# Performance work log

Measured on AMD Instinct MI355X. Metric: run time of the kernel, lower is better.

## Reference

```python
import jax, jax.numpy as jnp
import numpy as np

N = 16384      # nodes
E = 131072     # edges
L = 256        # latent size
H = 256        # mlp hidden size
S = 4          # message passing steps
OUT = 128      # decoder node output size
EPS = 1e-6     # flax LayerNorm epsilon


def _mlp(x, W0, b0, W1, b1):
    h = jax.nn.relu(x @ W0 + b0)
    return h @ W1 + b1


def _mlp_ln(x, W0, b0, W1, b1, ls, lb):
    y = _mlp(x, W0, b0, W1, b1)
    mu = y.mean(-1, keepdims=True)
    var = ((y - mu) ** 2).mean(-1, keepdims=True)
    return (y - mu) * jax.lax.rsqrt(var + EPS) * ls + lb


def setup_inputs() -> dict:
    key = jax.random.key(0)
    ks = iter(jax.random.split(key, 64))
    std = 0.02

    def w(shape):
        return jax.random.normal(next(ks), shape, dtype=jnp.float32) * std

    inp = {
        'node_feats': jax.random.normal(next(ks), (N, 3), dtype=jnp.float32),
        'edge_feats': jax.random.normal(next(ks), (E, 4), dtype=jnp.float32),
        'senders': jax.random.randint(next(ks), (E,), 0, N, dtype=jnp.int32),
        'receivers': jax.random.randint(next(ks), (E,), 0, N, dtype=jnp.int32),
        # node embedder MLP (3 -> H -> L) + LayerNorm
        'en_W0': w((3, H)), 'en_b0': jnp.zeros((H,)), 'en_W1': w((H, L)), 'en_b1': jnp.zeros((L,)),
        'en_ls': jnp.ones((L,)), 'en_lb': jnp.zeros((L,)),
        # edge embedder MLP (4 -> H -> L) + LayerNorm
        'ee_W0': w((4, H)), 'ee_b0': jnp.zeros((H,)), 'ee_W1': w((H, L)), 'ee_b1': jnp.zeros((L,)),
        'ee_ls': jnp.ones((L,)), 'ee_lb': jnp.zeros((L,)),
        # processor edge MLPs, stacked over S steps (3L -> H -> L) + LN
        'pe_W0': w((S, 3 * L, H)), 'pe_b0': jnp.zeros((S, H)), 'pe_W1': w((S, H, L)), 'pe_b1': jnp.zeros((S, L)),
        'pe_ls': jnp.ones((S, L)), 'pe_lb': jnp.zeros((S, L)),
        # processor node MLPs, stacked over S steps (2L -> H -> L) + LN
        'pn_W0': w((S, 2 * L, H)), 'pn_b0': jnp.zeros((S, H)), 'pn_W1': w((S, H, L)), 'pn_b1': jnp.zeros((S, L)),
        'pn_ls': jnp.ones((S, L)), 'pn_lb': jnp.zeros((S, L)),
        # node decoder MLP (L -> H -> OUT), no LayerNorm
        'dn_W0': w((L, H)), 'dn_b0': jnp.zeros((H,)), 'dn_W1': w((H, OUT)), 'dn_b1': jnp.zeros((OUT,)),
    }
    return inp


def reference(node_feats, edge_feats, senders, receivers,
              en_W0, en_b0, en_W1, en_b1, en_ls, en_lb,
              ee_W0, ee_b0, ee_W1, ee_b1, ee_ls, ee_lb,
              pe_W0, pe_b0, pe_W1, pe_b1, pe_ls, pe_lb,
              pn_W0, pn_b0, pn_W1, pn_b1, pn_ls, pn_lb,
              dn_W0, dn_b0, dn_W1, dn_b1):
    # Embed raw node/edge features into latent space.
    nodes = _mlp_ln(node_feats, en_W0, en_b0, en_W1, en_b1, en_ls, en_lb)   # [N, L]
    edges = _mlp_ln(edge_feats, ee_W0, ee_b0, ee_W1, ee_b1, ee_ls, ee_lb)   # [E, L]

    def step(carry, p):
        nodes, edges = carry
        (eW0, eb0, eW1, eb1, els, elb, nW0, nb0, nW1, nb1, nls, nlb) = p
        # Edge update: MLP on [edge, sender_node, receiver_node].
        ein = jnp.concatenate([edges, nodes[senders], nodes[receivers]], axis=-1)  # [E, 3L]
        new_e = _mlp_ln(ein, eW0, eb0, eW1, eb1, els, elb)                          # [E, L]
        # Aggregate new edge messages into receiver nodes (segment_sum).
        agg = jax.ops.segment_sum(new_e, receivers, num_segments=N)                # [N, L]
        # Node update: MLP on [node, aggregated messages].
        nin = jnp.concatenate([nodes, agg], axis=-1)                                # [N, 2L]
        new_n = _mlp_ln(nin, nW0, nb0, nW1, nb1, nls, nlb)                          # [N, L]
        # Residual connections (as in DeepTypedGraphNet processor).
        return (nodes + new_n, edges + new_e), None

    (nodes, edges), _ = jax.lax.scan(
        step, (nodes, edges),
        (pe_W0, pe_b0, pe_W1, pe_b1, pe_ls, pe_lb,
         pn_W0, pn_b0, pn_W1, pn_b1, pn_ls, pn_lb))

    # Decoder on nodes (no LayerNorm on the output head).
    out = _mlp(nodes, dn_W0, dn_b0, dn_W1, dn_b1)  # [N, OUT]
    return out
```

## Files before the change

kernel.cpp:

```cpp
#include <hip/hip_runtime.h>
#include <hip/hip_bf16.h>

#define NN 16384
#define NE 131072
#define L 256
#define SSTEPS 4
#define OUTD 128

typedef __attribute__((ext_vector_type(8))) short bf16x8;
typedef __attribute__((ext_vector_type(4))) float f32x4;

typedef const unsigned __attribute__((address_space(1)))* as1_u32p;
typedef unsigned __attribute__((address_space(3)))* as3_u32p;

__device__ __forceinline__ void gload16(const void* g, void* lds) {
  __builtin_amdgcn_global_load_lds((as1_u32p)g, (as3_u32p)lds, 16, 0, 0);
}

__device__ __forceinline__ short f2bs(float f) {
  unsigned u = __builtin_bit_cast(unsigned, f);
  u = (u + 0x7fffu + ((u >> 16) & 1u)) >> 16;
  return (short)u;
}
__device__ __forceinline__ float bs2f(short s) {
  unsigned u = ((unsigned)(unsigned short)s) << 16;
  return __builtin_bit_cast(float, u);
}
__device__ __forceinline__ unsigned cvt_pk_bf16(float lo, float hi) {
  unsigned r;
  asm("v_cvt_pk_bf16_f32 %0, %1, %2" : "=v"(r) : "v"(lo), "v"(hi));
  return r;
}
__device__ __forceinline__ bf16x8 pack_bf16x8(const float v[8]) {
  union { unsigned u[4]; bf16x8 b; } r;
#pragma unroll
  for (int k = 0; k < 4; ++k) r.u[k] = cvt_pk_bf16(v[2 * k], v[2 * k + 1]);
  return r.b;
}

__device__ __forceinline__ void store_tile(short* hs, int l, int mi, int nb,
                                           f32x4 v) {
  const int lm = l & 15, g = l >> 4;
#pragma unroll
  for (int i = 0; i < 4; ++i) {
    const float part = __shfl_xor(v[i], 1);
    if ((l & 1) == 0) {
      const int row = mi * 16 + g * 4 + i;
      const int col = nb + lm;
      const int off = (row * 512 + col * 2) ^ ((row & 7) << 4);
      *(unsigned*)((char*)hs + off) = cvt_pk_bf16(v[i], part);
    }
  }
}

template <int MI, int NT, int KC, int AST>
__device__ __forceinline__ void gemm_lds(const short* __restrict__ Wp,
                                         int Ncols, const short* hs, int n0,
                                         int l, f32x4 acc[MI][NT]) {
  const int lm = l & 15, g = l >> 4;
#pragma unroll
  for (int kc = 0; kc < KC; ++kc) {
    bf16x8 a[MI];
#pragma unroll
    for (int mi = 0; mi < MI; ++mi) {
      const int row = mi * 16 + lm;
      const int off = (row * AST + kc * 64 + g * 16) ^ ((row & 7) << 4);
      a[mi] = *(const bf16x8*)((const char*)hs + off);
    }
#pragma unroll
    for (int ni = 0; ni < NT; ++ni) {
      const int n = n0 + ni * 16 + lm;
      bf16x8 b = *(const bf16x8*)(Wp + ((size_t)kc * Ncols + n) * 32 + g * 8);
#pragma unroll
      for (int mi = 0; mi < MI; ++mi)
        acc[mi][ni] =
            __builtin_amdgcn_mfma_f32_16x16x32_bf16(a[mi], b, acc[mi][ni], 0, 0, 0);
    }
  }
}

__global__ void pack_w(const float* __restrict__ src, short* __restrict__ dst,
                       int K, int N, int cnt) {
  const size_t total = (size_t)K * N * cnt;
  for (size_t i = (size_t)blockIdx.x * blockDim.x + threadIdx.x; i < total;
       i += (size_t)gridDim.x * blockDim.x) {
    const size_t mat = i / ((size_t)K * N);
    const int rem = (int)(i - mat * (size_t)K * N);
    const int k = rem / N, n = rem - k * N;
    dst[mat * (size_t)K * N + ((size_t)(k >> 5) * N + n) * 32 + (k & 31)] =
        f2bs(src[i]);
  }
}

__global__ void pack_w0_pad(const float* __restrict__ src,
                            short* __restrict__ dst, int Kreal) {
  const int i = blockIdx.x * 256 + threadIdx.x;
  if (i >= 256 * 32) return;
  const int n = i >> 5, k = i & 31;
  dst[n * 32 + k] = (k < Kreal) ? f2bs(src[k * 256 + n]) : (short)0;
}

__device__ __forceinline__ void stage_tile256(const short* __restrict__ src0,
                                              short* As, int w, int l) {
#pragma unroll
  for (int i = 0; i < 4; ++i) {
    const int rbase = w * 8 + i * 2;
    const int r = rbase + (l >> 5);
    const int boff = ((l & 31) * 16) ^ ((r & 7) << 4);
    gload16((const char*)(src0 + (size_t)r * L) + boff, As + rbase * 256);
  }
}

__device__ __forceinline__ void stage_nodes_half16(
    const short* __restrict__ a_src, short* As, int w, int l, int n0) {
#pragma unroll
  for (int i = 0; i < 4; ++i) {
    const int r = w * 4 + i;
    if (l < 32) {
      const int cb = (l * 16) ^ ((r & 7) << 4);
      gload16((const char*)(a_src + (size_t)(n0 + r) * L) + cb, As + r * 512);
    }
  }
}

__global__ void csr_hist(const int* __restrict__ recv, int* __restrict__ deg) {
  const int e = blockIdx.x * 256 + threadIdx.x;
  atomicAdd(&deg[recv[e]], 1);
}
__global__ __launch_bounds__(256) void csr_scan(const int* __restrict__ deg,
                                                int* __restrict__ start,
                                                int* __restrict__ cursor) {
  __shared__ int part[256];
  const int t = threadIdx.x;
  int s = 0;
  for (int i = 0; i < NN / 256; ++i) s += deg[t * (NN / 256) + i];
  part[t] = s;
  __syncthreads();
  if (t == 0) {
    int acc = 0;
    for (int i = 0; i < 256; ++i) {
      const int v = part[i];
      part[i] = acc;
      acc += v;
    }
  }
  __syncthreads();
  int acc = part[t];
  for (int i = 0; i < NN / 256; ++i) {
    const int n = t * (NN / 256) + i;
    start[n] = acc;
    cursor[n] = acc;
    acc += deg[n];
  }
  if (t == 255) start[NN] = acc;
}
__global__ void csr_scatter(const int* __restrict__ recv,
                            int* __restrict__ cursor, int* __restrict__ elist) {
  const int e = blockIdx.x * 256 + threadIdx.x;
  const int p = atomicAdd(&cursor[recv[e]], 1);
  elist[p] = e;
}
__global__ void csr_sort(const int* __restrict__ start, int* __restrict__ elist) {
  const int n = blockIdx.x * blockDim.x + threadIdx.x;
  if (n >= NN) return;
  const int b = start[n], e = start[n + 1];
  for (int i = b + 1; i < e; ++i) {
    const int v = elist[i];
    int j = i - 1;
    while (j >= b && elist[j] > v) {
      elist[j + 1] = elist[j];
      --j;
    }
    elist[j + 1] = v;
  }
}

__device__ __forceinline__ void ln_row(const short* smem, int row, int seg,
                                       const float lsv[16], const float lbv[16],
                                       float ne[16]) {
  const int off0 = (row * 512 + seg * 16) ^ ((row & 7) << 4);
  const int off1 = (row * 512 + 256 + seg * 16) ^ ((row & 7) << 4);
  const bf16x8 y0 = *(const bf16x8*)((const char*)smem + off0);
  const bf16x8 y1 = *(const bf16x8*)((const char*)smem + off1);
  float v[16];
#pragma unroll
  for (int k = 0; k < 8; ++k) {
    v[k] = bs2f(y0[k]);
    v[8 + k] = bs2f(y1[k]);
  }
  float s = 0.f;
#pragma unroll
  for (int k = 0; k < 16; ++k) s += v[k];
#pragma unroll
  for (int o = 1; o < 16; o <<= 1) s += __shfl_xor(s, o);
  const float mu = s * (1.f / 256.f);
  float sq = 0.f;
#pragma unroll
  for (int k = 0; k < 16; ++k) {
    const float d = v[k] - mu;
    sq += d * d;
  }
#pragma unroll
  for (int o = 1; o < 16; o <<= 1) sq += __shfl_xor(sq, o);
  const float rstd = rsqrtf(sq * (1.f / 256.f) + 1e-6f);
#pragma unroll
  for (int k = 0; k < 16; ++k) ne[k] = (v[k] - mu) * rstd * lsv[k] + lbv[k];
}

__device__ __forceinline__ void load16(const float* __restrict__ p, int seg,
                                       float d[16]) {
  const float4 a0 = *(const float4*)(p + seg * 8);
  const float4 a1 = *(const float4*)(p + seg * 8 + 4);
  const float4 a2 = *(const float4*)(p + 128 + seg * 8);
  const float4 a3 = *(const float4*)(p + 128 + seg * 8 + 4);
  d[0] = a0.x; d[1] = a0.y; d[2] = a0.z; d[3] = a0.w;
  d[4] = a1.x; d[5] = a1.y; d[6] = a1.z; d[7] = a1.w;
  d[8] = a2.x; d[9] = a2.y; d[10] = a2.z; d[11] = a2.w;
  d[12] = a3.x; d[13] = a3.y; d[14] = a3.z; d[15] = a3.w;
}

__global__ __launch_bounds__(256, 4) void proj_mfma(
    const short* __restrict__ nodes_b, const short* __restrict__ Wfull,
    short* __restrict__ NSb, short* __restrict__ NRb) {
  __shared__ char smem[16384];
  short* As = (short*)smem;
  const int t = threadIdx.x, w = t >> 6, l = t & 63;
  const int tr = t >> 4, seg = t & 15;
  const int n0 = blockIdx.x * 32;
  const short* Wp = Wfull + (size_t)(8 + blockIdx.y * 8) * 256 * 32;
  short* out = blockIdx.y ? NRb : NSb;

  stage_tile256(nodes_b + (size_t)n0 * L, As, w, l);
  __syncthreads();

  f32x4 acc[2][4] = {};
  gemm_lds<2, 4, 8, 512>(Wp, L, As, w * 64, l, acc);
  __syncthreads();
#pragma unroll
  for (int ni = 0; ni < 4; ++ni)
#pragma unroll
    for (int mi = 0; mi < 2; ++mi)
      store_tile(As, l, mi, w * 64 + ni * 16, acc[mi][ni]);
  __syncthreads();

#pragma unroll
  for (int p = 0; p < 2; ++p) {
    const int row = p * 16 + tr;
    const int off0 = (row * 512 + seg * 16) ^ ((row & 7) << 4);
    const int off1 = (row * 512 + 256 + seg * 16) ^ ((row & 7) << 4);
    *(bf16x8*)(out + (size_t)(n0 + row) * L + seg * 8) =
        *(const bf16x8*)((const char*)As + off0);
    *(bf16x8*)(out + (size_t)(n0 + row) * L + 128 + seg * 8) =
        *(const bf16x8*)((const char*)As + off1);
  }
}

__global__ __launch_bounds__(256, 4) void edge_step_mfma(
    const short* __restrict__ NSb, const short* __restrict__ NRb,
    short* __restrict__ edges_b, short* __restrict__ new_e,
    const int* __restrict__ senders, const int* __restrict__ receivers,
    const short* __restrict__ W0p, const float* __restrict__ b0,
    const short* __restrict__ W1p, const float* __restrict__ b1,
    const float* __restrict__ ls, const float* __restrict__ lb) {
  __shared__ char smem[32768];
  short* As = (short*)smem;
  short* nsrB = (short*)(smem + 16384);
  const int t = threadIdx.x, w = t >> 6, l = t & 63;
  const int lm = l & 15, g = l >> 4;
  const int tr = t >> 4, seg = t & 15;
  const int e0 = blockIdx.x * 32;

  const int sn0 = senders[e0 + tr], rc0 = receivers[e0 + tr];
  const int sn1 = senders[e0 + 16 + tr], rc1 = receivers[e0 + 16 + tr];
  stage_tile256(edges_b + (size_t)e0 * L, As, w, l);
  __syncthreads();

  bf16x8 gn[2][2], gr[2][2];
  {
    const short* p0 = NSb + (size_t)sn0 * L + seg * 8;
    gn[0][0] = *(const bf16x8*)p0;
    gn[0][1] = *(const bf16x8*)(p0 + 128);
    const short* p1 = NSb + (size_t)sn1 * L + seg * 8;
    gn[1][0] = *(const bf16x8*)p1;
    gn[1][1] = *(const bf16x8*)(p1 + 128);
    const short* q0 = NRb + (size_t)rc0 * L + seg * 8;
    gr[0][0] = *(const bf16x8*)q0;
    gr[0][1] = *(const bf16x8*)(q0 + 128);
    const short* q1 = NRb + (size_t)rc1 * L + seg * 8;
    gr[1][0] = *(const bf16x8*)q1;
    gr[1][1] = *(const bf16x8*)(q1 + 128);
  }

  f32x4 acc[2][4] = {};
  gemm_lds<2, 4, 8, 512>(W0p, L, As, w * 64, l, acc);

  bf16x8 old0[2], old1[2];
#pragma unroll
  for (int p = 0; p < 2; ++p) {
    const int row = p * 16 + tr;
    old0[p] = *(const bf16x8*)((const char*)As +
                               ((row * 512 + seg * 16) ^ ((row & 7) << 4)));
    old1[p] = *(const bf16x8*)((const char*)As +
                               ((row * 512 + 256 + seg * 16) ^ ((row & 7) << 4)));
  }

#pragma unroll
  for (int p = 0; p < 2; ++p) {
    const int row = p * 16 + tr;
    float s[16];
#pragma unroll
    for (int k = 0; k < 8; ++k) {
      s[k] = bs2f(gn[p][0][k]) + bs2f(gr[p][0][k]);
      s[8 + k] = bs2f(gn[p][1][k]) + bs2f(gr[p][1][k]);
    }
    const int off0 = (row * 512 + seg * 16) ^ ((row & 7) << 4);
    const int off1 = (row * 512 + 256 + seg * 16) ^ ((row & 7) << 4);
    *(bf16x8*)((char*)nsrB + off0) = pack_bf16x8(s);
    *(bf16x8*)((char*)nsrB + off1) = pack_bf16x8(s + 8);
  }
  __syncthreads();

#pragma unroll
  for (int ni = 0; ni < 4; ++ni) {
    const float bia = b0[w * 64 + ni * 16 + lm];
    const int col = w * 64 + ni * 16 + lm;
#pragma unroll
    for (int mi = 0; mi < 2; ++mi) {
      f32x4 v = acc[mi][ni];
#pragma unroll
      for (int i = 0; i < 4; ++i) {
        const int row = mi * 16 + g * 4 + i;
        const int noff = (row * 512 + col * 2) ^ ((row & 7) << 4);
        v[i] = fmaxf(v[i] + bia + bs2f(*(const short*)((const char*)nsrB + noff)),
                     0.f);
      }
      store_tile(As, l, mi, w * 64 + ni * 16, v);
    }
  }
  __syncthreads();

  f32x4 acc2[2][4] = {};
  gemm_lds<2, 4, 8, 512>(W1p, L, As, w * 64, l, acc2);
#pragma unroll
  for (int ni = 0; ni < 4; ++ni) {
    const float bia = b1[w * 64 + ni * 16 + lm];
#pragma unroll
    for (int mi = 0; mi < 2; ++mi) {
      f32x4 v = acc2[mi][ni];
#pragma unroll
      for (int i = 0; i < 4; ++i) v[i] += bia;
      store_tile(nsrB, l, mi, w * 64 + ni * 16, v);
    }
  }
  __syncthreads();

  float lsv[16], lbv[16];
  load16(ls, seg, lsv);
  load16(lb, seg, lbv);
#pragma unroll
  for (int p = 0; p < 2; ++p) {
    const int row = p * 16 + tr;
    float ne[16];
    ln_row(nsrB, row, seg, lsv, lbv, ne);
    const size_t e = (size_t)(e0 + row);
    *(bf16x8*)(new_e + e * L + seg * 8) = pack_bf16x8(ne);
    *(bf16x8*)(new_e + e * L + 128 + seg * 8) = pack_bf16x8(ne + 8);
    float r0[8], r1[8];
#pragma unroll
    for (int k = 0; k < 8; ++k) {
      r0[k] = bs2f(old0[p][k]) + ne[k];
      r1[k] = bs2f(old1[p][k]) + ne[8 + k];
    }
    *(bf16x8*)(edges_b + e * L + seg * 8) = pack_bf16x8(r0);
    *(bf16x8*)(edges_b + e * L + 128 + seg * 8) = pack_bf16x8(r1);
  }
}

__global__ __launch_bounds__(256, 4) void node_step_mfma(
    float* __restrict__ nodes_f, short* __restrict__ nodes_b,
    const short* __restrict__ new_e, const int* __restrict__ start,
    const int* __restrict__ elist, const short* __restrict__ W0p,
    const float* __restrict__ b0, const short* __restrict__ W1p,
    const float* __restrict__ b1, const float* __restrict__ ls,
    const float* __restrict__ lb, const short* __restrict__ W0nS,
    const short* __restrict__ W0nR, short* __restrict__ NSb,
    short* __restrict__ NRb) {
  __shared__ char smem[16384];
  short* As = (short*)smem;
  short* hb = (short*)smem;
  short* yb = (short*)(smem + 8192);
  const int t = threadIdx.x, w = t >> 6, l = t & 63;
  const int lm = l & 15;
  const int tr = t >> 4, seg = t & 15;
  const int n0 = blockIdx.x * 16;

  stage_nodes_half16(nodes_b, As, w, l, n0);

  {
    const int grp = t >> 5, lc = t & 31;
#pragma unroll
    for (int i = 0; i < 2; ++i) {
      const int r = grp * 2 + i;
      const int n = n0 + r;
      const int b = start[n], e = start[n + 1];
      float acc[8] = {0.f, 0.f, 0.f, 0.f, 0.f, 0.f, 0.f, 0.f};
      if (b < e) {
        bf16x8 v = *(const bf16x8*)(new_e + (size_t)elist[b] * L + lc * 8);
        for (int j = b + 1; j < e; ++j) {
          const bf16x8 nx =
              *(const bf16x8*)(new_e + (size_t)elist[j] * L + lc * 8);
#pragma unroll
          for (int k = 0; k < 8; ++k) acc[k] += bs2f(v[k]);
          v = nx;
        }
#pragma unroll
        for (int k = 0; k < 8; ++k) acc[k] += bs2f(v[k]);
      }
      const int off = (r * 1024 + 512 + lc * 16) ^ ((r & 7) << 4);
      *(bf16x8*)((char*)As + off) = pack_bf16x8(acc);
    }
  }
  __syncthreads();

  f32x4 acc[1][4] = {};
  gemm_lds<1, 4, 16, 1024>(W0p, L, As, w * 64, l, acc);
  __syncthreads();

#pragma unroll
  for (int ni = 0; ni < 4; ++ni) {
    const float bia = b0[w * 64 + ni * 16 + lm];
    f32x4 v = acc[0][ni];
#pragma unroll
    for (int i = 0; i < 4; ++i) v[i] = fmaxf(v[i] + bia, 0.f);
    store_tile(hb, l, 0, w * 64 + ni * 16, v);
  }
  __syncthreads();

  f32x4 acc2[1][4] = {};
  gemm_lds<1, 4, 8, 512>(W1p, L, hb, w * 64, l, acc2);
  __syncthreads();
#pragma unroll
  for (int ni = 0; ni < 4; ++ni) {
    const float bia = b1[w * 64 + ni * 16 + lm];
    f32x4 v = acc2[0][ni];
#pragma unroll
    for (int i = 0; i < 4; ++i) v[i] += bia;
    store_tile(yb, l, 0, w * 64 + ni * 16, v);
  }
  __syncthreads();

  float lsv[16], lbv[16];
  load16(ls, seg, lsv);
  load16(lb, seg, lbv);
  {
    const int row = tr;
    float ne[16];
    ln_row(yb, row, seg, lsv, lbv, ne);
    const size_t n = (size_t)(n0 + row);
    float* nf = nodes_f + n * L;
    float fv[16];
    load16(nf, seg, fv);
    float nv[16];
#pragma unroll
    for (int k = 0; k < 16; ++k) nv[k] = fv[k] + ne[k];
    *(float4*)(nf + seg * 8) = make_float4(nv[0], nv[1], nv[2], nv[3]);
    *(float4*)(nf + seg * 8 + 4) = make_float4(nv[4], nv[5], nv[6], nv[7]);
    *(float4*)(nf + 128 + seg * 8) = make_float4(nv[8], nv[9], nv[10], nv[11]);
    *(float4*)(nf + 128 + seg * 8 + 4) = make_float4(nv[12], nv[13], nv[14], nv[15]);
    const bf16x8 nb0 = pack_bf16x8(nv);
    const bf16x8 nb1 = pack_bf16x8(nv + 8);
    *(bf16x8*)(nodes_b + n * L + seg * 8) = nb0;
    *(bf16x8*)(nodes_b + n * L + 128 + seg * 8) = nb1;
    const int off0 = (row * 512 + seg * 16) ^ ((row & 7) << 4);
    const int off1 = (row * 512 + 256 + seg * 16) ^ ((row & 7) << 4);
    *(bf16x8*)((char*)hb + off0) = nb0;
    *(bf16x8*)((char*)hb + off1) = nb1;
  }

  if (W0nS == nullptr) return;
  __syncthreads();

  {
    f32x4 pa[1][4] = {};
    gemm_lds<1, 4, 8, 512>(W0nS, L, hb, w * 64, l, pa);
#pragma unroll
    for (int ni = 0; ni < 4; ++ni)
      store_tile(yb, l, 0, w * 64 + ni * 16, pa[0][ni]);
    __syncthreads();
    {
      const int row = tr;
      const int off0 = (row * 512 + seg * 16) ^ ((row & 7) << 4);
      const int off1 = (row * 512 + 256 + seg * 16) ^ ((row & 7) << 4);
      *(bf16x8*)(NSb + (size_t)(n0 + row) * L + seg * 8) =
          *(const bf16x8*)((const char*)yb + off0);
      *(bf16x8*)(NSb + (size_t)(n0 + row) * L + 128 + seg * 8) =
          *(const bf16x8*)((const char*)yb + off1);
    }
  }
  __syncthreads();

  {
    f32x4 pa[1][4] = {};
    gemm_lds<1, 4, 8, 512>(W0nR, L, hb, w * 64, l, pa);
#pragma unroll
    for (int ni = 0; ni < 4; ++ni)
      store_tile(yb, l, 0, w * 64 + ni * 16, pa[0][ni]);
    __syncthreads();
    {
      const int row = tr;
      const int off0 = (row * 512 + seg * 16) ^ ((row & 7) << 4);
      const int off1 = (row * 512 + 256 + seg * 16) ^ ((row & 7) << 4);
      *(bf16x8*)(NRb + (size_t)(n0 + row) * L + seg * 8) =
          *(const bf16x8*)((const char*)yb + off0);
      *(bf16x8*)(NRb + (size_t)(n0 + row) * L + 128 + seg * 8) =
          *(const bf16x8*)((const char*)yb + off1);
    }
  }
}

template <int K1, bool WF32>
__global__ __launch_bounds__(256) void embed_mfma(
    const float* __restrict__ x, const short* __restrict__ W0p,
    const float* __restrict__ b0, const short* __restrict__ W1p,
    const float* __restrict__ b1, const float* __restrict__ ls,
    const float* __restrict__ lb, float* __restrict__ dst_f,
    short* __restrict__ dst_b) {
  __shared__ short hs[64 * 256];
  __shared__ short xsb[64 * 32];
  const int t = threadIdx.x, w = t >> 6, l = t & 63;
  const int lm = l & 15, g = l >> 4;
  const int tr = t >> 4, seg = t & 15;
  const int r0 = blockIdx.x * 64;

  if (t < 64) {
    const float* xr = x + (size_t)(r0 + t) * K1;
    float v[8] = {0.f, 0.f, 0.f, 0.f, 0.f, 0.f, 0.f, 0.f};
#pragma unroll
    for (int k = 0; k < K1; ++k) v[k] = xr[k];
    bf16x8 z;
#pragma unroll
    for (int k = 0; k < 8; ++k) z[k] = 0;
    char* rb = (char*)xsb + t * 64;
    *(bf16x8*)(rb + (0 ^ ((t & 3) << 4))) = pack_bf16x8(v);
#pragma unroll
    for (int gi = 1; gi < 4; ++gi) *(bf16x8*)(rb + ((gi * 16) ^ ((t & 3) << 4))) = z;
  }
  __syncthreads();

  f32x4 acc[4][4] = {};
  {
    bf16x8 a[4];
#pragma unroll
    for (int mi = 0; mi < 4; ++mi) {
      const int row = mi * 16 + lm;
      a[mi] = *(const bf16x8*)((const char*)xsb + row * 64 +
                               ((g * 16) ^ ((row & 3) << 4)));
    }
#pragma unroll
    for (int ni = 0; ni < 4; ++ni) {
      const int n = w * 64 + ni * 16 + lm;
      bf16x8 b = *(const bf16x8*)(W0p + n * 32 + g * 8);
#pragma unroll
      for (int mi = 0; mi < 4; ++mi)
        acc[mi][ni] =
            __builtin_amdgcn_mfma_f32_16x16x32_bf16(a[mi], b, acc[mi][ni], 0, 0, 0);
    }
  }
#pragma unroll
  for (int ni = 0; ni < 4; ++ni) {
    const float bia = b0[w * 64 + ni * 16 + lm];
#pragma unroll
    for (int mi = 0; mi < 4; ++mi) {
      f32x4 v = acc[mi][ni];
#pragma unroll
      for (int i = 0; i < 4; ++i) v[i] = fmaxf(v[i] + bia, 0.f);
      store_tile(hs, l, mi, w * 64 + ni * 16, v);
    }
  }
  __syncthreads();

  f32x4 acc2[4][4] = {};
  gemm_lds<4, 4, 8, 512>(W1p, L, hs, w * 64, l, acc2);
  __syncthreads();
#pragma unroll
  for (int ni = 0; ni < 4; ++ni) {
    const float bia = b1[w * 64 + ni * 16 + lm];
#pragma unroll
    for (int mi = 0; mi < 4; ++mi) {
      f32x4 v = acc2[mi][ni];
#pragma unroll
      for (int i = 0; i < 4; ++i) v[i] += bia;
      store_tile(hs, l, mi, w * 64 + ni * 16, v);
    }
  }
  __syncthreads();

  float lsv[16], lbv[16];
  load16(ls, seg, lsv);
  load16(lb, seg, lbv);
#pragma unroll
  for (int p = 0; p < 4; ++p) {
    const int row = p * 16 + tr;
    float ne[16];
    ln_row(hs, row, seg, lsv, lbv, ne);
    const size_t n = (size_t)(r0 + row);
    *(bf16x8*)(dst_b + n * L + seg * 8) = pack_bf16x8(ne);
    *(bf16x8*)(dst_b + n * L + 128 + seg * 8) = pack_bf16x8(ne + 8);
    if (WF32) {
      float* df = dst_f + n * L;
      *(float4*)(df + seg * 8) = make_float4(ne[0], ne[1], ne[2], ne[3]);
      *(float4*)(df + seg * 8 + 4) = make_float4(ne[4], ne[5], ne[6], ne[7]);
      *(float4*)(df + 128 + seg * 8) = make_float4(ne[8], ne[9], ne[10], ne[11]);
      *(float4*)(df + 128 + seg * 8 + 4) =
          make_float4(ne[12], ne[13], ne[14], ne[15]);
    }
  }
}

__global__ __launch_bounds__(256) void decoder_mfma(
    const short* __restrict__ nodes_b, const short* __restrict__ W0p,
    const float* __restrict__ b0, const short* __restrict__ W1p,
    const float* __restrict__ b1, float* __restrict__ out) {
  __shared__ short hs[64 * 256];
  const int t = threadIdx.x, w = t >> 6, l = t & 63;
  const int lm = l & 15, g = l >> 4;
  const int n0 = blockIdx.x * 64;

  const short* baseA[4];
#pragma unroll
  for (int mi = 0; mi < 4; ++mi)
    baseA[mi] = nodes_b + (size_t)(n0 + mi * 16 + lm) * L;

  f32x4 acc[4][4] = {};
#pragma unroll
  for (int kc = 0; kc < 8; ++kc) {
    const int koff = kc * 32 + g * 8;
    bf16x8 a[4];
#pragma unroll
    for (int mi = 0; mi < 4; ++mi) a[mi] = *(const bf16x8*)(baseA[mi] + koff);
#pragma unroll
    for (int ni = 0; ni < 4; ++ni) {
      const int n = w * 64 + ni * 16 + lm;
      bf16x8 b = *(const bf16x8*)(W0p + ((size_t)kc * L + n) * 32 + g * 8);
#pragma unroll
      for (int mi = 0; mi < 4; ++mi)
        acc[mi][ni] = __builtin_amdgcn_mfma_f32_16x16x32_bf16(a[mi], b,
                                                             acc[mi][ni],
                                                             0, 0, 0);
    }
  }
#pragma unroll
  for (int ni = 0; ni < 4; ++ni) {
    const float bia = b0[w * 64 + ni * 16 + lm];
#pragma unroll
    for (int mi = 0; mi < 4; ++mi) {
      f32x4 v = acc[mi][ni];
#pragma unroll
      for (int i = 0; i < 4; ++i) v[i] = fmaxf(v[i] + bia, 0.f);
      store_tile(hs, l, mi, w * 64 + ni * 16, v);
    }
  }
  __syncthreads();

  f32x4 acc2[4][2] = {};
  gemm_lds<4, 2, 8, 512>(W1p, OUTD, hs, w * 32, l, acc2);

  float b14[2];
#pragma unroll
  for (int ni = 0; ni < 2; ++ni) b14[ni] = b1[w * 32 + ni * 16 + lm];
#pragma unroll
  for (int mi = 0; mi < 4; ++mi)
#pragma unroll
    for (int ni = 0; ni < 2; ++ni)
#pragma unroll
      for (int i = 0; i < 4; ++i) {
        const int row = n0 + mi * 16 + g * 4 + i;
        const int col = w * 32 + ni * 16 + lm;
        out[(size_t)row * OUTD + col] = acc2[mi][ni][i] + b14[ni];
      }
}

extern "C" void kernel_launch(void* const* d_in, const int* in_sizes, int n_in,
                              void* d_out, int out_size, void* d_ws,
                              size_t ws_size, hipStream_t stream) {
  const float* node_feats = (const float*)d_in[0];
  const float* edge_feats = (const float*)d_in[1];
  const int* senders = (const int*)d_in[2];
  const int* receivers = (const int*)d_in[3];
  auto f = [&](int i) { return (const float*)d_in[i]; };

  char* p = (char*)d_ws;
  auto alloc = [&](size_t bytes) {
    char* q = p;
    p += (bytes + 255) & ~(size_t)255;
    return q;
  };
  float* nodes_f = (float*)alloc((size_t)NN * L * 4);
  short* nodes_b = (short*)alloc((size_t)NN * L * 2);
  short* edges_b = (short*)alloc((size_t)NE * L * 2);
  short* new_e = (short*)alloc((size_t)NE * L * 2);
  short* NSb = (short*)alloc((size_t)NN * L * 2);
  short* NRb = (short*)alloc((size_t)NN * L * 2);
  int* deg = (int*)alloc((size_t)NN * 4);
  int* start = (int*)alloc((size_t)(NN + 16) * 4);
  int* cursor = (int*)alloc((size_t)NN * 4);
  int* elist = (int*)alloc((size_t)NE * 4);
  short* en_W0p = (short*)alloc(256 * 32 * 2);
  short* ee_W0p = (short*)alloc(256 * 32 * 2);
  short* en_W1p = (short*)alloc(65536 * 2);
  short* ee_W1p = (short*)alloc(65536 * 2);
  short* pe_W0p = (short*)alloc((size_t)4 * 768 * 256 * 2);
  short* pe_W1p = (short*)alloc((size_t)4 * 65536 * 2);
  short* pn_W0p = (short*)alloc((size_t)4 * 512 * 256 * 2);
  short* pn_W1p = (short*)alloc((size_t)4 * 65536 * 2);
  short* dn_W0p = (short*)alloc(65536 * 2);
  short* dn_W1p = (short*)alloc(32768 * 2);

  hipMemsetAsync(deg, 0, (size_t)NN * 4, stream);
  csr_hist<<<NE / 256, 256, 0, stream>>>(receivers, deg);
  csr_scan<<<1, 256, 0, stream>>>(deg, start, cursor);
  csr_scatter<<<NE / 256, 256, 0, stream>>>(receivers, cursor, elist);
  csr_sort<<<NN / 256, 256, 0, stream>>>(start, elist);

  pack_w0_pad<<<32, 256, 0, stream>>>(f(4), en_W0p, 3);
  pack_w0_pad<<<32, 256, 0, stream>>>(f(10), ee_W0p, 4);
  pack_w<<<256, 256, 0, stream>>>(f(6), en_W1p, 256, 256, 1);
  pack_w<<<256, 256, 0, stream>>>(f(12), ee_W1p, 256, 256, 1);
  pack_w<<<1024, 256, 0, stream>>>(f(16), pe_W0p, 768, 256, 4);
  pack_w<<<512, 256, 0, stream>>>(f(18), pe_W1p, 256, 256, 4);
  pack_w<<<1024, 256, 0, stream>>>(f(22), pn_W0p, 512, 256, 4);
  pack_w<<<512, 256, 0, stream>>>(f(24), pn_W1p, 256, 256, 4);
  pack_w<<<256, 256, 0, stream>>>(f(28), dn_W0p, 256, 256, 1);
  pack_w<<<128, 256, 0, stream>>>(f(30), dn_W1p, 256, 128, 1);

  embed_mfma<3, true><<<NN / 64, 256, 0, stream>>>(
      node_feats, en_W0p, f(5), en_W1p, f(7), f(8), f(9), nodes_f, nodes_b);
  embed_mfma<4, false><<<NE / 64, 256, 0, stream>>>(
      edge_feats, ee_W0p, f(11), ee_W1p, f(13), f(14), f(15), nullptr, edges_b);

  for (int s = 0; s < SSTEPS; ++s) {
    const short* W0s = pe_W0p + (size_t)s * 768 * 256;
    if (s == 0)
      proj_mfma<<<dim3(NN / 32, 2), 256, 0, stream>>>(nodes_b, W0s, NSb, NRb);
    edge_step_mfma<<<NE / 32, 256, 0, stream>>>(
        NSb, NRb, edges_b, new_e, senders, receivers, W0s,
        f(17) + (size_t)s * 256, pe_W1p + (size_t)s * 65536,
        f(19) + (size_t)s * 256, f(20) + (size_t)s * 256,
        f(21) + (size_t)s * 256);
    const short* W0n = (s + 1 < SSTEPS) ? pe_W0p + (size_t)(s + 1) * 768 * 256
                                        : nullptr;
    node_step_mfma<<<NN / 16, 256, 0, stream>>>(
        nodes_f, nodes_b, new_e, start, elist,
        pn_W0p + (size_t)s * 512 * 256, f(23) + (size_t)s * 256,
        pn_W1p + (size_t)s * 65536, f(25) + (size_t)s * 256,
        f(26) + (size_t)s * 256, f(27) + (size_t)s * 256,
        W0n ? W0n + (size_t)8 * 256 * 32 : nullptr,
        W0n ? W0n + (size_t)16 * 256 * 32 : nullptr, NSb, NRb);
  }

  decoder_mfma<<<NN / 64, 256, 0, stream>>>(nodes_b, dn_W0p, f(29), dn_W1p,
                                            f(31), (float*)d_out);
}
```

Baseline: 811.1 us.

## Store edges in receiver-sorted order so aggregation reads contiguous rows

Edges are permuted into CSR (receiver-sorted) order once: edge embeddings are gathered through elist, and the sender/receiver arrays are permuted to match. Each edge-step then writes new_e in sorted order, so the node-step segment sum reads contiguous rows instead of indirecting through elist. Edge state stays consistent because it only ever lives in permuted order. This adds a small permutation kernel and an indexed read in the edge embedder.

```diff
diff --git a/kernel.cpp b/kernel.cpp
--- a/kernel.cpp
+++ b/kernel.cpp
@@ -173,6 +173,15 @@
     }
     elist[j + 1] = v;
   }
+}
+__global__ void permute_se(const int* __restrict__ elist,
+                           const int* __restrict__ senders,
+                           const int* __restrict__ receivers,
+                           int* __restrict__ sn_p, int* __restrict__ rc_p) {
+  const int p = blockIdx.x * 256 + threadIdx.x;
+  const int e = elist[p];
+  sn_p[p] = senders[e];
+  rc_p[p] = receivers[e];
 }
 
 __device__ __forceinline__ void ln_row(const short* smem, int row, int seg,
@@ -379,12 +388,11 @@
 __global__ __launch_bounds__(256, 4) void node_step_mfma(
     float* __restrict__ nodes_f, short* __restrict__ nodes_b,
     const short* __restrict__ new_e, const int* __restrict__ start,
-    const int* __restrict__ elist, const short* __restrict__ W0p,
-    const float* __restrict__ b0, const short* __restrict__ W1p,
-    const float* __restrict__ b1, const float* __restrict__ ls,
-    const float* __restrict__ lb, const short* __restrict__ W0nS,
-    const short* __restrict__ W0nR, short* __restrict__ NSb,
-    short* __restrict__ NRb) {
+    const short* __restrict__ W0p, const float* __restrict__ b0,
+    const short* __restrict__ W1p, const float* __restrict__ b1,
+    const float* __restrict__ ls, const float* __restrict__ lb,
+    const short* __restrict__ W0nS, const short* __restrict__ W0nR,
+    short* __restrict__ NSb, short* __restrict__ NRb) {
   __shared__ char smem[16384];
   short* As = (short*)smem;
   short* hb = (short*)smem;
@@ -404,15 +412,8 @@
       const int n = n0 + r;
       const int b = start[n], e = start[n + 1];
       float acc[8] = {0.f, 0.f, 0.f, 0.f, 0.f, 0.f, 0.f, 0.f};
-      if (b < e) {
-        bf16x8 v = *(const bf16x8*)(new_e + (size_t)elist[b] * L + lc * 8);
-        for (int j = b + 1; j < e; ++j) {
-          const bf16x8 nx =
-              *(const bf16x8*)(new_e + (size_t)elist[j] * L + lc * 8);
-#pragma unroll
-          for (int k = 0; k < 8; ++k) acc[k] += bs2f(v[k]);
-          v = nx;
-        }
+      for (int j = b; j < e; ++j) {
+        const bf16x8 v = *(const bf16x8*)(new_e + (size_t)j * L + lc * 8);
 #pragma unroll
         for (int k = 0; k < 8; ++k) acc[k] += bs2f(v[k]);
       }
@@ -520,11 +521,11 @@
 
 template <int K1, bool WF32>
 __global__ __launch_bounds__(256) void embed_mfma(
-    const float* __restrict__ x, const short* __restrict__ W0p,
-    const float* __restrict__ b0, const short* __restrict__ W1p,
-    const float* __restrict__ b1, const float* __restrict__ ls,
-    const float* __restrict__ lb, float* __restrict__ dst_f,
-    short* __restrict__ dst_b) {
+    const float* __restrict__ x, const int* __restrict__ gidx,
+    const short* __restrict__ W0p, const float* __restrict__ b0,
+    const short* __restrict__ W1p, const float* __restrict__ b1,
+    const float* __restrict__ ls, const float* __restrict__ lb,
+    float* __restrict__ dst_f, short* __restrict__ dst_b) {
   __shared__ short hs[64 * 256];
   __shared__ short xsb[64 * 32];
   const int t = threadIdx.x, w = t >> 6, l = t & 63;
@@ -533,7 +534,8 @@
   const int r0 = blockIdx.x * 64;
 
   if (t < 64) {
-    const float* xr = x + (size_t)(r0 + t) * K1;
+    const size_t srow = gidx ? (size_t)gidx[r0 + t] : (size_t)(r0 + t);
+    const float* xr = x + srow * K1;
     float v[8] = {0.f, 0.f, 0.f, 0.f, 0.f, 0.f, 0.f, 0.f};
 #pragma unroll
     for (int k = 0; k < K1; ++k) v[k] = xr[k];
@@ -705,6 +707,8 @@
   int* start = (int*)alloc((size_t)(NN + 16) * 4);
   int* cursor = (int*)alloc((size_t)NN * 4);
   int* elist = (int*)alloc((size_t)NE * 4);
+  int* sn_p = (int*)alloc((size_t)NE * 4);
+  int* rc_p = (int*)alloc((size_t)NE * 4);
   short* en_W0p = (short*)alloc(256 * 32 * 2);
   short* ee_W0p = (short*)alloc(256 * 32 * 2);
   short* en_W1p = (short*)alloc(65536 * 2);
@@ -721,6 +725,8 @@
   csr_scan<<<1, 256, 0, stream>>>(deg, start, cursor);
   csr_scatter<<<NE / 256, 256, 0, stream>>>(receivers, cursor, elist);
   csr_sort<<<NN / 256, 256, 0, stream>>>(start, elist);
+  permute_se<<<NE / 256, 256, 0, stream>>>(elist, senders, receivers, sn_p,
+                                           rc_p);
 
   pack_w0_pad<<<32, 256, 0, stream>>>(f(4), en_W0p, 3);
   pack_w0_pad<<<32, 256, 0, stream>>>(f(10), ee_W0p, 4);
@@ -734,27 +740,27 @@
   pack_w<<<128, 256, 0, stream>>>(f(30), dn_W1p, 256, 128, 1);
 
   embed_mfma<3, true><<<NN / 64, 256, 0, stream>>>(
-      node_feats, en_W0p, f(5), en_W1p, f(7), f(8), f(9), nodes_f, nodes_b);
+      node_feats, nullptr, en_W0p, f(5), en_W1p, f(7), f(8), f(9), nodes_f,
+      nodes_b);
   embed_mfma<4, false><<<NE / 64, 256, 0, stream>>>(
-      edge_feats, ee_W0p, f(11), ee_W1p, f(13), f(14), f(15), nullptr, edges_b);
+      edge_feats, elist, ee_W0p, f(11), ee_W1p, f(13), f(14), f(15), nullptr,
+      edges_b);
 
   for (int s = 0; s < SSTEPS; ++s) {
     const short* W0s = pe_W0p + (size_t)s * 768 * 256;
     if (s == 0)
       proj_mfma<<<dim3(NN / 32, 2), 256, 0, stream>>>(nodes_b, W0s, NSb, NRb);
     edge_step_mfma<<<NE / 32, 256, 0, stream>>>(
-        NSb, NRb, edges_b, new_e, senders, receivers, W0s,
-        f(17) + (size_t)s * 256, pe_W1p + (size_t)s * 65536,
-        f(19) + (size_t)s * 256, f(20) + (size_t)s * 256,
-        f(21) + (size_t)s * 256);
+        NSb, NRb, edges_b, new_e, sn_p, rc_p, W0s, f(17) + (size_t)s * 256,
+        pe_W1p + (size_t)s * 65536, f(19) + (size_t)s * 256,
+        f(20) + (size_t)s * 256, f(21) + (size_t)s * 256);
     const short* W0n = (s + 1 < SSTEPS) ? pe_W0p + (size_t)(s + 1) * 768 * 256
                                         : nullptr;
     node_step_mfma<<<NN / 16, 256, 0, stream>>>(
-        nodes_f, nodes_b, new_e, start, elist,
-        pn_W0p + (size_t)s * 512 * 256, f(23) + (size_t)s * 256,
-        pn_W1p + (size_t)s * 65536, f(25) + (size_t)s * 256,
-        f(26) + (size_t)s * 256, f(27) + (size_t)s * 256,
-        W0n ? W0n + (size_t)8 * 256 * 32 : nullptr,
+        nodes_f, nodes_b, new_e, start, pn_W0p + (size_t)s * 512 * 256,
+        f(23) + (size_t)s * 256, pn_W1p + (size_t)s * 65536,
+        f(25) + (size_t)s * 256, f(26) + (size_t)s * 256,
+        f(27) + (size_t)s * 256, W0n ? W0n + (size_t)8 * 256 * 32 : nullptr,
         W0n ? W0n + (size_t)16 * 256 * 32 : nullptr, NSb, NRb);
   }
 
```

After: 806.6 us (median of 2 runs). Within noise of the previous version (-0.5%).
